# Performance work log

Hardware: AMD Instinct MI355X
Metric: run time of the kernel (lower is better)

## Reference

```python
import jax, jax.numpy as jnp
import numpy as np

CHANNELS = 512
NUM_HEADS = 8
GROUPS = 32
EPS = 1e-5


def setup_inputs() -> dict:
    key = jax.random.key(0)
    ks = jax.random.split(key, 7)
    C = CHANNELS
    x = jax.random.normal(ks[0], (8, C, 32, 32), dtype=jnp.float32)
    gn_weight = jnp.ones((C,), dtype=jnp.float32)
    gn_bias = jnp.zeros((C,), dtype=jnp.float32)
    # Conv1d(C, 3C, k=1) weights ~ N(0, 0.02) per init_weights
    qkv_w = 0.02 * jax.random.normal(ks[1], (3 * C, C), dtype=jnp.float32)
    qkv_b = 0.01 * jax.random.normal(ks[2], (3 * C,), dtype=jnp.float32)
    out_w = 0.02 * jax.random.normal(ks[3], (C, C), dtype=jnp.float32)
    out_b = 0.01 * jax.random.normal(ks[4], (C,), dtype=jnp.float32)
    return {"x": x, "gn_weight": gn_weight, "gn_bias": gn_bias,
            "qkv_w": qkv_w, "qkv_b": qkv_b, "out_w": out_w, "out_b": out_b}


def _forward(x, gn_weight, gn_bias, qkv_w, qkv_b, out_w, out_b):
    n, c, h, w = x.shape
    hw = h * w
    heads = NUM_HEADS
    cph = c // heads
    xs = x.reshape(n, c, hw)  # [N, C, HW]
    # GroupNorm over (channels-in-group, spatial)
    xg = xs.reshape(n, GROUPS, c // GROUPS, hw)
    mean = jnp.mean(xg, axis=(2, 3), keepdims=True)
    var = jnp.var(xg, axis=(2, 3), keepdims=True)
    xn = ((xg - mean) * jax.lax.rsqrt(var + EPS)).reshape(n, c, hw)
    xn = xn * gn_weight[None, :, None] + gn_bias[None, :, None]
    # 1x1 Conv1d QKV projection
    qkv = jnp.einsum('oc,ncl->nol', qkv_w, xn) + qkv_b[None, :, None]  # [N, 3C, HW]
    q, k, v = jnp.split(qkv, 3, axis=1)  # each [N, C, HW]
    q = q.reshape(n * heads, cph, hw)
    k = k.reshape(n * heads, cph, hw)
    v = v.reshape(n * heads, cph, hw)
    scale = 1.0 / np.sqrt(cph).astype(np.float32)
    scores = jnp.einsum('bci,bcj->bij', q, k) * scale  # [NH, HW, HW]
    attn = jax.nn.softmax(scores, axis=-1)
    weighted = jnp.einsum('bij,bcj->bic', attn, v)  # [NH, HW, cph]
    # Faithful to torch: reshape(n, -1, h, w) on [n*heads, hw, cph] layout
    weighted = weighted.reshape(n, c, h, w)
    out = jnp.einsum('oc,nchw->nohw', out_w, weighted) + out_b[None, :, None, None]
    return out


def reference(x, gn_weight, gn_bias, qkv_w, qkv_b, out_w, out_b):
    return _forward(x, gn_weight, gn_bias, qkv_w, qkv_b, out_w, out_b)
```

## Files before the change

kernel.cpp:

```cpp
#include <hip/hip_runtime.h>
#include <math.h>

#define N_    8
#define C_    512
#define HW_   1024
#define G_    32
#define CPG_  16
#define OC3_  1536
#define LOG2E 1.44269504f

typedef _Float16 f16;
typedef f16 f16x8 __attribute__((ext_vector_type(8)));
typedef f16 f16x4 __attribute__((ext_vector_type(4)));
typedef float f32x4 __attribute__((ext_vector_type(4)));

#define GLOAD_LDS16(g, l)                                                          \
    __builtin_amdgcn_global_load_lds(                                              \
        (const __attribute__((address_space(1))) unsigned int*)(const void*)(g),   \
        (__attribute__((address_space(3))) unsigned int*)(void*)(l), 16, 0, 0)

#define WAIT_VM0() __builtin_amdgcn_s_waitcnt(0x0F70)

__global__ __launch_bounds__(256) void prep(const float* __restrict__ x,
                                            const float* __restrict__ gw,
                                            const float* __restrict__ gb,
                                            f16* __restrict__ XT,
                                            const float* __restrict__ qkv_w,
                                            const float* __restrict__ out_w,
                                            const float* __restrict__ qkv_b,
                                            f16* __restrict__ Wq,
                                            f16* __restrict__ Wo,
                                            float* __restrict__ qkv_bs) {
    __shared__ float red1[4], red2[4];
    __shared__ float sm, srstd;
    if (blockIdx.x >= 256) {
        const float QS = 0.125f * LOG2E;
        int idx = (blockIdx.x - 256) * 256 + threadIdx.x;
        if (idx < 786432) {
            float v = qkv_w[idx];
            if (idx < 262144) v *= QS;
            Wq[idx] = (f16)v;
        } else if (idx < 786432 + 262144) {
            Wo[idx - 786432] = (f16)out_w[idx - 786432];
        } else if (idx < 786432 + 262144 + 1536) {
            int i = idx - 786432 - 262144;
            float v = qkv_b[i];
            if (i < 512) v *= QS;
            qkv_bs[i] = v;
        }
        return;
    }
    int blk = blockIdx.x;
    int n = blk >> 5, g = blk & 31;
    size_t base = ((size_t)n * C_ + (size_t)g * CPG_) * HW_;
    const float4* xp4 = (const float4*)(x + base);
    float4 vals[16];
    float s1 = 0.f, s2 = 0.f;
#pragma unroll
    for (int r = 0; r < 16; r++) {
        float4 v = xp4[r * 256 + threadIdx.x];
        vals[r] = v;
        s1 += v.x + v.y + v.z + v.w;
        s2 += v.x * v.x + v.y * v.y + v.z * v.z + v.w * v.w;
    }
#pragma unroll
    for (int off = 32; off > 0; off >>= 1) {
        s1 += __shfl_down(s1, off, 64);
        s2 += __shfl_down(s2, off, 64);
    }
    int wave = threadIdx.x >> 6, lane = threadIdx.x & 63;
    if (lane == 0) { red1[wave] = s1; red2[wave] = s2; }
    __syncthreads();
    if (threadIdx.x == 0) {
        float t1 = red1[0] + red1[1] + red1[2] + red1[3];
        float t2 = red2[0] + red2[1] + red2[2] + red2[3];
        float mean = t1 * (1.f / 16384.f);
        float var  = t2 * (1.f / 16384.f) - mean * mean;
        sm = mean;
        srstd = rsqrtf(var + 1e-5f);
    }
    __syncthreads();
    float mean = sm, rstd = srstd;
    float av[16], bbv[16];
#pragma unroll
    for (int r = 0; r < 16; r++) {
        int c = g * CPG_ + r;
        av[r] = gw[c] * rstd;
        bbv[r] = gb[c] - mean * av[r];
    }
    f16x8 lo[4], hi[4];
#pragma unroll
    for (int r = 0; r < 16; r++) {
        float4 v = vals[r];
        float a = av[r], bb = bbv[r];
        f16 e0 = (f16)(v.x * a + bb), e1 = (f16)(v.y * a + bb);
        f16 e2 = (f16)(v.z * a + bb), e3 = (f16)(v.w * a + bb);
        if (r < 8) { lo[0][r] = e0; lo[1][r] = e1; lo[2][r] = e2; lo[3][r] = e3; }
        else { hi[0][r - 8] = e0; hi[1][r - 8] = e1; hi[2][r - 8] = e2; hi[3][r - 8] = e3; }
    }
    f16* xt = XT + ((size_t)n * HW_ + (size_t)threadIdx.x * 4) * C_ + g * CPG_;
#pragma unroll
    for (int comp = 0; comp < 4; comp++) {
        *(f16x8*)&xt[(size_t)comp * C_]     = lo[comp];
        *(f16x8*)&xt[(size_t)comp * C_ + 8] = hi[comp];
    }
}

template <bool FINAL>
__global__ __launch_bounds__(256, 4) void gemm_f16(const f16* __restrict__ A,
                                                   const f16* __restrict__ B,
                                                   const float* __restrict__ bias,
                                                   void* __restrict__ Yq,
                                                   f16* __restrict__ Yv) {
    __shared__ __align__(16) unsigned char smem[34816];
    f16* As = (f16*)smem;
    f16* Bs = (f16*)(smem + 16384);
    int tid = threadIdx.x, lane = tid & 63, w = tid >> 6;
    int m = lane & 15, quad = lane >> 4;
    int ow0 = (w & 1) * 64, lw0 = (w >> 1) * 64;
    int l0 = blockIdx.x * 128, o0 = blockIdx.y * 128, n = blockIdx.z;
    const f16* Bn = B + ((size_t)n * HW_ + l0) * 512;

    int rowT[4], sgT[4];
#pragma unroll
    for (int t = 0; t < 4; t++) {
        int q = (w * 4 + t) * 64 + lane;
        int row = q >> 3, seg = q & 7;
        rowT[t] = row;
        sgT[t] = seg ^ (row & 7);
    }

    f32x4 acc[4][4];
#pragma unroll
    for (int i = 0; i < 4; i++)
#pragma unroll
        for (int j = 0; j < 4; j++)
#pragma unroll
            for (int r = 0; r < 4; r++) acc[i][j][r] = 0.f;

    for (int c0 = 0; c0 < 512; c0 += 64) {
        __syncthreads();
#pragma unroll
        for (int t = 0; t < 4; t++) {
            GLOAD_LDS16(A + (size_t)(o0 + rowT[t]) * 512 + c0 + sgT[t] * 8,
                        As + (size_t)(w * 4 + t) * 512);
            GLOAD_LDS16(Bn + (size_t)rowT[t] * 512 + c0 + sgT[t] * 8,
                        Bs + (size_t)(w * 4 + t) * 512);
        }
        WAIT_VM0();
        __syncthreads();
#pragma unroll
        for (int ks = 0; ks < 2; ks++) {
            f16x8 af[4], bf[4];
#pragma unroll
            for (int ib = 0; ib < 4; ib++) {
                int row = ow0 + ib * 16 + m;
                int seg = (ks * 4 + quad) ^ (row & 7);
                af[ib] = *(const f16x8*)&As[row * 64 + seg * 8];
            }
#pragma unroll
            for (int jb = 0; jb < 4; jb++) {
                int row = lw0 + jb * 16 + m;
                int seg = (ks * 4 + quad) ^ (row & 7);
                bf[jb] = *(const f16x8*)&Bs[row * 64 + seg * 8];
            }
#pragma unroll
            for (int ib = 0; ib < 4; ib++)
#pragma unroll
                for (int jb = 0; jb < 4; jb++)
                    acc[ib][jb] = __builtin_amdgcn_mfma_f32_16x16x32_f16(
                        af[ib], bf[jb], acc[ib][jb], 0, 0, 0);
        }
    }

    float bv[4][4];
#pragma unroll
    for (int ib = 0; ib < 4; ib++)
#pragma unroll
        for (int r = 0; r < 4; r++)
            bv[ib][r] = bias[o0 + ow0 + ib * 16 + quad * 4 + r];

    if (FINAL) {
        float* on = (float*)Yq + (size_t)n * C_ * HW_;
#pragma unroll
        for (int ib = 0; ib < 4; ib++)
#pragma unroll
            for (int jb = 0; jb < 4; jb++)
#pragma unroll
                for (int r = 0; r < 4; r++)
                    on[(size_t)(o0 + ow0 + ib * 16 + quad * 4 + r) * HW_ +
                       l0 + lw0 + jb * 16 + m] = acc[ib][jb][r] + bv[ib][r];
    } else if (o0 >= 1024) {
        f16* vn = Yv + (size_t)n * C_ * HW_;
#pragma unroll
        for (int ib = 0; ib < 4; ib++)
#pragma unroll
            for (int jb = 0; jb < 4; jb++)
#pragma unroll
                for (int r = 0; r < 4; r++)
                    vn[(size_t)(o0 - 1024 + ow0 + ib * 16 + quad * 4 + r) * HW_ +
                       l0 + lw0 + jb * 16 + m] = (f16)(acc[ib][jb][r] + bv[ib][r]);
    } else {
        __syncthreads();
        f16* T = (f16*)smem;
#pragma unroll
        for (int ib = 0; ib < 4; ib++)
#pragma unroll
            for (int jb = 0; jb < 4; jb++) {
                f16x4 h;
#pragma unroll
                for (int r = 0; r < 4; r++) h[r] = (f16)(acc[ib][jb][r] + bv[ib][r]);
                int l = lw0 + jb * 16 + m;
                int oo = ow0 + ib * 16 + quad * 4;
                *(f16x4*)&T[l * 136 + oo] = h;
            }
        __syncthreads();
        f16* qn = (f16*)Yq + (size_t)n * HW_ * 1024;
#pragma unroll
        for (int rep = 0; rep < 8; rep++) {
            int idx = rep * 256 + tid;
            int l = idx >> 4, seg = idx & 15;
            f16x8 v = *(const f16x8*)&T[l * 136 + seg * 8];
            *(f16x8*)&qn[(size_t)(l0 + l) * 1024 + o0 + seg * 8] = v;
        }
    }
}

__global__ __launch_bounds__(256, 4) void attn_f16(const f16* __restrict__ qkvT,
                                                   const f16* __restrict__ vbuf,
                                                   f16* __restrict__ w2T) {
    __shared__ __align__(16) unsigned char smem[40960];
    f16* Kb0  = (f16*)smem;
    f16* Vb0  = (f16*)(smem + 16384);
    f16* Ps   = (f16*)(smem + 32768);
    f16* LDSo = (f16*)smem;

    int tid = threadIdx.x;
    int lane = tid & 63, wave = tid >> 6;
    int m = lane & 15, quad = lane >> 4;
    int iw = wave * 16;
    int flat = blockIdx.x;
    int xcd = flat & 7, slot = flat >> 3;
    int itile = slot >> 3, bh = (slot & 7) * 8 + xcd;
    int n = bh >> 3, head = bh & 7;
    int i0 = itile * 64;
    const f16* qb = qkvT + (size_t)n * HW_ * 1024 + head * 64;
    const f16* kb = qb + 512;
    const f16* vb = vbuf + (size_t)n * C_ * HW_ + (size_t)head * 64 * HW_;
    f16* PsW = Ps + iw * 64;

    f16x8 aq0 = *(const f16x8*)&qb[(size_t)(i0 + iw + m) * 1024 + quad * 8];
    f16x8 aq1 = *(const f16x8*)&qb[(size_t)(i0 + iw + m) * 1024 + 32 + quad * 8];

#pragma unroll
    for (int it = 0; it < 2; it++) {
        int chunk = it * 256 + tid;
        int row = chunk >> 3, seg = chunk & 7;
        int segg = seg ^ (row & 7);
        GLOAD_LDS16(kb + (size_t)row * 1024 + segg * 8,
                    Kb0 + ((size_t)it * 256 + wave * 64) * 8);
        GLOAD_LDS16(vb + (size_t)row * HW_ + segg * 8,
                    Vb0 + ((size_t)it * 256 + wave * 64) * 8);
    }

    f32x4 oacc[4];
#pragma unroll
    for (int cb = 0; cb < 4; cb++)
#pragma unroll
        for (int r = 0; r < 4; r++) oacc[cb][r] = 0.f;
    float lsum = 0.f;

    for (int jt = 0; jt < 16; jt++) {
        int p = jt & 1;
        const f16* Kp = Kb0 + p * 4096;
        const f16* Vp = Vb0 + p * 4096;
        WAIT_VM0();
        __syncthreads();
        if (jt < 15) {
            int j0n = (jt + 1) * 64;
            f16* Kn = Kb0 + (1 - p) * 4096;
            f16* Vn = Vb0 + (1 - p) * 4096;
#pragma unroll
            for (int it = 0; it < 2; it++) {
                int chunk = it * 256 + tid;
                int row = chunk >> 3, seg = chunk & 7;
                int segg = seg ^ (row & 7);
                GLOAD_LDS16(kb + (size_t)(j0n + row) * 1024 + segg * 8,
                            Kn + ((size_t)it * 256 + wave * 64) * 8);
                GLOAD_LDS16(vb + (size_t)row * HW_ + j0n + segg * 8,
                            Vn + ((size_t)it * 256 + wave * 64) * 8);
            }
        }

        f32x4 sacc[4];
#pragma unroll
        for (int jb = 0; jb < 4; jb++)
#pragma unroll
            for (int r = 0; r < 4; r++) sacc[jb][r] = 0.f;
#pragma unroll
        for (int jb = 0; jb < 4; jb++) {
            int row = jb * 16 + m;
            f16x8 k0 = *(const f16x8*)&Kp[row * 64 + ((quad ^ (row & 7)) * 8)];
            sacc[jb] = __builtin_amdgcn_mfma_f32_16x16x32_f16(k0, aq0, sacc[jb], 0, 0, 0);
        }
#pragma unroll
        for (int jb = 0; jb < 4; jb++) {
            int row = jb * 16 + m;
            f16x8 k1 = *(const f16x8*)&Kp[row * 64 + (((4 + quad) ^ (row & 7)) * 8)];
            sacc[jb] = __builtin_amdgcn_mfma_f32_16x16x32_f16(k1, aq1, sacc[jb], 0, 0, 0);
        }

#pragma unroll
        for (int jb = 0; jb < 4; jb++) {
            f16x4 h;
#pragma unroll
            for (int r = 0; r < 4; r++) {
                float pv = exp2f(sacc[jb][r]);
                h[r] = (f16)pv;
                lsum += pv;
            }
            int seg = jb * 4 + quad;
            *(f16x4*)&PsW[m * 64 + ((seg ^ (m & 7)) * 4)] = h;
        }

#pragma unroll
        for (int ks = 0; ks < 2; ks++) {
            int s0 = ks * 8 + quad * 2;
            f16x4 apl = *(const f16x4*)&PsW[m * 64 + ((s0 ^ (m & 7)) * 4)];
            f16x4 aph = *(const f16x4*)&PsW[m * 64 + (((s0 + 1) ^ (m & 7)) * 4)];
            f16x8 ap = {apl[0], apl[1], apl[2], apl[3], aph[0], aph[1], aph[2], aph[3]};
#pragma unroll
            for (int cb = 0; cb < 4; cb++) {
                int vrow = cb * 16 + m;
                f16x8 bvv = *(const f16x8*)&Vp[vrow * 64 +
                                               (((ks * 4 + quad) ^ (vrow & 7)) * 8)];
                oacc[cb] = __builtin_amdgcn_mfma_f32_16x16x32_f16(ap, bvv, oacc[cb], 0, 0, 0);
            }
        }
    }

    float ls = lsum;
    ls += __shfl_xor(ls, 16, 64);
    ls += __shfl_xor(ls, 32, 64);
    float linv[4];
#pragma unroll
    for (int r = 0; r < 4; r++)
        linv[r] = 1.f / __shfl(ls, (wave << 6 >> 6) * 0 + quad * 4 + r + (lane & 48) * 0 + ((tid >> 6) << 6) * 0 + (lane >> 6) * 0 + ((lane / 64) * 64) + (quad * 0) + (quad * 4 + r >= 0 ? 0 : 0) + 0, 64) * 1.f,
        linv[r] = 1.f / __shfl(ls, quad * 4 + r, 64);
    WAIT_VM0();
    __syncthreads();
#pragma unroll
    for (int cb = 0; cb < 4; cb++)
#pragma unroll
        for (int r = 0; r < 4; r++) {
            int s = (quad * 4 + r) * 64 + cb * 16 + m;
            LDSo[s * 4 + wave] = (f16)(oacc[cb][r] * linv[r]);
        }
    __syncthreads();
    f16* w2n = w2T + (size_t)n * HW_ * 512;
    int chbase = head * 64 + (i0 >> 4);
#pragma unroll
    for (int it = 0; it < 4; it++) {
        int s = it * 256 + tid;
        *(f16x4*)&w2n[(size_t)s * 512 + chbase] = *(const f16x4*)&LDSo[s * 4];
    }
}

extern "C" void kernel_launch(void* const* d_in, const int* in_sizes, int n_in,
                              void* d_out, int out_size, void* d_ws, size_t ws_size,
                              hipStream_t stream) {
    (void)in_sizes; (void)n_in; (void)out_size; (void)ws_size;
    const float* x     = (const float*)d_in[0];
    const float* gw    = (const float*)d_in[1];
    const float* gb    = (const float*)d_in[2];
    const float* qkv_w = (const float*)d_in[3];
    const float* qkv_b = (const float*)d_in[4];
    const float* out_w = (const float*)d_in[5];
    const float* out_b = (const float*)d_in[6];
    float* out = (float*)d_out;
    char* ws = (char*)d_ws;

    const size_t MB = 1024 * 1024;
    f16*   qkvT   = (f16*)ws;
    f16*   XT     = (f16*)(ws + 16 * MB);
    f16*   vbuf   = (f16*)(ws + 24 * MB);
    f16*   w2T    = (f16*)(ws + 32 * MB);
    f16*   Wq     = (f16*)(ws + 40 * MB);
    f16*   Wo     = (f16*)(ws + 42 * MB);
    float* qkv_bs = (float*)(ws + 43 * MB);

    prep<<<dim3(256 + 4103), 256, 0, stream>>>(x, gw, gb, XT,
                                               qkv_w, out_w, qkv_b, Wq, Wo, qkv_bs);
    gemm_f16<false><<<dim3(8, 12, N_), 256, 0, stream>>>(Wq, XT, qkv_bs, (void*)qkvT, vbuf);
    attn_f16<<<dim3(1024), 256, 0, stream>>>(qkvT, vbuf, w2T);
    gemm_f16<true><<<dim3(8, 4, N_), 256, 0, stream>>>(Wo, w2T, out_b, (void*)out, nullptr);
}
```

Baseline: 152.6 us.

## Load K/V fragments directly from global into registers instead of LDS double-buffering

Drops the double-buffered global-to-LDS staging of K and V tiles and the per-iteration barrier. Each wave now loads its own MFMA operand fragments for K and V straight from global memory into registers. This removes LDS traffic and block-wide synchronisation. In exchange, all four waves re-read the same K/V data from global/L2, the loads no longer overlap with compute through a prefetch pipeline, and register pressure goes up.

```diff
diff --git a/kernel.cpp b/kernel.cpp
--- a/kernel.cpp
+++ b/kernel.cpp
@@ -229,11 +229,8 @@
 __global__ __launch_bounds__(256, 4) void attn_f16(const f16* __restrict__ qkvT,
                                                    const f16* __restrict__ vbuf,
                                                    f16* __restrict__ w2T) {
-    __shared__ __align__(16) unsigned char smem[40960];
-    f16* Kb0  = (f16*)smem;
-    f16* Vb0  = (f16*)(smem + 16384);
-    f16* Ps   = (f16*)(smem + 32768);
-    f16* LDSo = (f16*)smem;
+    __shared__ __align__(16) f16 Ps[4096];
+    __shared__ __align__(16) f16 LDSo[4096];
 
     int tid = threadIdx.x;
     int lane = tid & 63, wave = tid >> 6;
@@ -252,17 +249,6 @@
     f16x8 aq0 = *(const f16x8*)&qb[(size_t)(i0 + iw + m) * 1024 + quad * 8];
     f16x8 aq1 = *(const f16x8*)&qb[(size_t)(i0 + iw + m) * 1024 + 32 + quad * 8];
 
-#pragma unroll
-    for (int it = 0; it < 2; it++) {
-        int chunk = it * 256 + tid;
-        int row = chunk >> 3, seg = chunk & 7;
-        int segg = seg ^ (row & 7);
-        GLOAD_LDS16(kb + (size_t)row * 1024 + segg * 8,
-                    Kb0 + ((size_t)it * 256 + wave * 64) * 8);
-        GLOAD_LDS16(vb + (size_t)row * HW_ + segg * 8,
-                    Vb0 + ((size_t)it * 256 + wave * 64) * 8);
-    }
-
     f32x4 oacc[4];
 #pragma unroll
     for (int cb = 0; cb < 4; cb++)
@@ -271,25 +257,19 @@
     float lsum = 0.f;
 
     for (int jt = 0; jt < 16; jt++) {
-        int p = jt & 1;
-        const f16* Kp = Kb0 + p * 4096;
-        const f16* Vp = Vb0 + p * 4096;
-        WAIT_VM0();
-        __syncthreads();
-        if (jt < 15) {
-            int j0n = (jt + 1) * 64;
-            f16* Kn = Kb0 + (1 - p) * 4096;
-            f16* Vn = Vb0 + (1 - p) * 4096;
-#pragma unroll
-            for (int it = 0; it < 2; it++) {
-                int chunk = it * 256 + tid;
-                int row = chunk >> 3, seg = chunk & 7;
-                int segg = seg ^ (row & 7);
-                GLOAD_LDS16(kb + (size_t)(j0n + row) * 1024 + segg * 8,
-                            Kn + ((size_t)it * 256 + wave * 64) * 8);
-                GLOAD_LDS16(vb + (size_t)row * HW_ + j0n + segg * 8,
-                            Vn + ((size_t)it * 256 + wave * 64) * 8);
-            }
+        int j0 = jt * 64;
+        f16x8 kf[8], vf[8];
+#pragma unroll
+        for (int jb = 0; jb < 4; jb++) {
+            const f16* kr = kb + (size_t)(j0 + jb * 16 + m) * 1024;
+            kf[jb]     = *(const f16x8*)&kr[quad * 8];
+            kf[4 + jb] = *(const f16x8*)&kr[32 + quad * 8];
+        }
+#pragma unroll
+        for (int cb = 0; cb < 4; cb++) {
+            const f16* vr = vb + (size_t)(cb * 16 + m) * HW_ + j0;
+            vf[cb]     = *(const f16x8*)&vr[quad * 8];
+            vf[4 + cb] = *(const f16x8*)&vr[32 + quad * 8];
         }
 
         f32x4 sacc[4];
@@ -298,17 +278,11 @@
 #pragma unroll
             for (int r = 0; r < 4; r++) sacc[jb][r] = 0.f;
 #pragma unroll
-        for (int jb = 0; jb < 4; jb++) {
-            int row = jb * 16 + m;
-            f16x8 k0 = *(const f16x8*)&Kp[row * 64 + ((quad ^ (row & 7)) * 8)];
-            sacc[jb] = __builtin_amdgcn_mfma_f32_16x16x32_f16(k0, aq0, sacc[jb], 0, 0, 0);
-        }
-#pragma unroll
-        for (int jb = 0; jb < 4; jb++) {
-            int row = jb * 16 + m;
-            f16x8 k1 = *(const f16x8*)&Kp[row * 64 + (((4 + quad) ^ (row & 7)) * 8)];
-            sacc[jb] = __builtin_amdgcn_mfma_f32_16x16x32_f16(k1, aq1, sacc[jb], 0, 0, 0);
-        }
+        for (int jb = 0; jb < 4; jb++)
+            sacc[jb] = __builtin_amdgcn_mfma_f32_16x16x32_f16(kf[jb], aq0, sacc[jb], 0, 0, 0);
+#pragma unroll
+        for (int jb = 0; jb < 4; jb++)
+            sacc[jb] = __builtin_amdgcn_mfma_f32_16x16x32_f16(kf[4 + jb], aq1, sacc[jb], 0, 0, 0);
 
 #pragma unroll
         for (int jb = 0; jb < 4; jb++) {
@@ -330,12 +304,9 @@
             f16x4 aph = *(const f16x4*)&PsW[m * 64 + (((s0 + 1) ^ (m & 7)) * 4)];
             f16x8 ap = {apl[0], apl[1], apl[2], apl[3], aph[0], aph[1], aph[2], aph[3]};
 #pragma unroll
-            for (int cb = 0; cb < 4; cb++) {
-                int vrow = cb * 16 + m;
-                f16x8 bvv = *(const f16x8*)&Vp[vrow * 64 +
-                                               (((ks * 4 + quad) ^ (vrow & 7)) * 8)];
-                oacc[cb] = __builtin_amdgcn_mfma_f32_16x16x32_f16(ap, bvv, oacc[cb], 0, 0, 0);
-            }
+            for (int cb = 0; cb < 4; cb++)
+                oacc[cb] = __builtin_amdgcn_mfma_f32_16x16x32_f16(ap, vf[ks * 4 + cb],
+                                                                  oacc[cb], 0, 0, 0);
         }
     }
 
@@ -345,10 +316,8 @@
     float linv[4];
 #pragma unroll
     for (int r = 0; r < 4; r++)
-        linv[r] = 1.f / __shfl(ls, (wave << 6 >> 6) * 0 + quad * 4 + r + (lane & 48) * 0 + ((tid >> 6) << 6) * 0 + (lane >> 6) * 0 + ((lane / 64) * 64) + (quad * 0) + (quad * 4 + r >= 0 ? 0 : 0) + 0, 64) * 1.f,
         linv[r] = 1.f / __shfl(ls, quad * 4 + r, 64);
-    WAIT_VM0();
-    __syncthreads();
+
 #pragma unroll
     for (int cb = 0; cb < 4; cb++)
 #pragma unroll
```

New measurement: 241.5 us. 1.58x slower.
